# Performance work log

Hardware: AMD Instinct MI355X
Metric: run time of the kernel (lower is better)

## Reference

```python
import jax, jax.numpy as jnp
import numpy as np
import math

B, S, D = 2, 2048, 1024
H = 16
HD = D // H
FFN = 2048
E = 8
TOP_K = 2
CAP_FACTOR = 1.25
EPS = 1e-6
BASE = 10000.0
CAP = max(math.ceil(B * S * TOP_K * CAP_FACTOR / E), 1)  # 1280


def setup_inputs() -> dict:
    key = jax.random.key(0)
    ks = jax.random.split(key, 6)
    sd = 0.02
    return {
        "x": jax.random.normal(ks[0], (B, S, D), jnp.float32),
        "g1": jnp.ones((D,), jnp.float32),
        "w_qkv": jax.random.normal(ks[1], (D, 3 * D), jnp.float32) * sd,
        "w_o": jax.random.normal(ks[2], (D, D), jnp.float32) * sd,
        "g2": jnp.ones((D,), jnp.float32),
        "w_router": jax.random.normal(ks[3], (D, E), jnp.float32) * sd,
        "w1": jax.random.normal(ks[4], (E, D, FFN), jnp.float32) * sd,
        "w2": jax.random.normal(ks[5], (E, FFN, D), jnp.float32) * sd,
    }


def _rmsnorm(x, w):
    rms = jax.lax.rsqrt(jnp.mean(x * x, axis=-1, keepdims=True) + EPS)
    return w * x * rms


def _rope(x, cos, sin):
    # x: [b,h,s,hd]; consecutive pairs (2i, 2i+1) form complex numbers
    xr = x[..., 0::2]
    xi = x[..., 1::2]
    c = cos[None, None]  # [1,1,s,hd/2]
    s_ = sin[None, None]
    out_r = xr * c - xi * s_
    out_i = xr * s_ + xi * c
    return jnp.stack([out_r, out_i], axis=-1).reshape(x.shape)


def _mha(x, w_qkv, w_o):
    b, s, d = x.shape
    qkv = x @ w_qkv
    q, k, v = jnp.split(qkv, 3, axis=-1)
    to_heads = lambda z: z.reshape(b, s, H, HD).transpose(0, 2, 1, 3)
    q, k, v = to_heads(q), to_heads(k), to_heads(v)
    # rotary embedding
    theta = BASE ** (-2.0 * (jnp.arange(HD // 2, dtype=jnp.float32) / HD))
    freqs = jnp.arange(s, dtype=jnp.float32)[:, None] * theta[None, :]  # [s,hd/2]
    cos, sin = jnp.cos(freqs), jnp.sin(freqs)
    q = _rope(q, cos, sin)
    k = _rope(k, cos, sin)
    scores = jnp.einsum('bhqd,bhkd->bhqk', q, k) / jnp.sqrt(jnp.float32(HD))
    causal = jnp.tril(jnp.ones((s, s), dtype=bool))
    scores = jnp.where(causal, scores, -jnp.inf)
    attn = jax.nn.softmax(scores, axis=-1)
    y = jnp.einsum('bhqk,bhkd->bhqd', attn, v)
    y = y.transpose(0, 2, 1, 3).reshape(b, s, d)
    return y @ w_o


def _moe(x, w_router, w1, w2):
    b, s, d = x.shape
    t = b * s
    xf = x.reshape(t, d)
    logits = xf.astype(jnp.float32) @ w_router.astype(jnp.float32)
    probs = jax.nn.softmax(logits, axis=-1)  # [t,E]
    g, eidx = jax.lax.top_k(probs, TOP_K)  # [t,K]
    fg = g.reshape(t * TOP_K)
    fe = eidx.reshape(t * TOP_K)
    tok_of = jnp.arange(t * TOP_K) // TOP_K
    # per-expert masked gates, then capacity-based top-CAP selection
    masked = jnp.where(fe[None, :] == jnp.arange(E)[:, None], fg[None, :], -jnp.inf)  # [E, t*K]
    vals, idx = jax.lax.top_k(masked, CAP)  # [E, CAP]
    valid = jnp.isfinite(vals)
    gates = jnp.where(valid, vals, 0.0)  # dropped/empty slots get zero gate
    tok = tok_of[idx]  # [E, CAP] token ids (arbitrary for invalid slots, gate 0)
    xe = xf[tok]  # [E, CAP, d]
    h = jax.nn.relu(jnp.einsum('ecd,edf->ecf', xe, w1))
    ye = jnp.einsum('ecf,efd->ecd', h, w2) * gates[..., None]
    y = jnp.zeros_like(xf).at[tok.reshape(-1)].add(ye.reshape(-1, d))
    return y.reshape(b, s, d)


def reference(x, g1, w_qkv, w_o, g2, w_router, w1, w2):
    x = x + _mha(_rmsnorm(x, g1), w_qkv, w_o)
    x = x + _moe(_rmsnorm(x, g2), w_router, w1, w2)
    return x
```

## Files before the change

kernel.cpp:

```cpp
#include <hip/hip_runtime.h>
#include <math.h>


#define B_   2
#define S_   2048
#define D_   1024
#define H_   16
#define HD_  64
#define FFN_ 2048
#define E_   8
#define CAP_ 1280
#define T_   (B_*S_)
#define NSLOT_ 72

typedef unsigned short u16;
typedef __attribute__((ext_vector_type(8))) short     short8;
typedef __attribute__((ext_vector_type(8))) _Float16  half8;
typedef __attribute__((ext_vector_type(4))) _Float16  half4;
typedef __attribute__((ext_vector_type(8))) unsigned short ushort8v;
typedef __attribute__((ext_vector_type(4))) float     f32x4;

__device__ __forceinline__ u16 f2bf(float f) {
  unsigned u = __float_as_uint(f);
  return (u16)((u + 0x7fffu + ((u >> 16) & 1u)) >> 16);
}
__device__ __forceinline__ float bf2f(u16 h) {
  return __uint_as_float(((unsigned)h) << 16);
}
__device__ __forceinline__ u16 f2h(float f) {
  _Float16 h = (_Float16)f;
  return __builtin_bit_cast(u16, h);
}
__device__ __forceinline__ float h2f(u16 b) {
  return (float)__builtin_bit_cast(_Float16, b);
}

__device__ __forceinline__ void cstore(float* p, float v) { *p = v; }
__device__ __forceinline__ void cstore(u16* p, float v)   { *p = f2bf(v); }

__device__ __forceinline__ void glds16(const u16* g, u16* l) {
  __builtin_amdgcn_global_load_lds(
      (const __attribute__((address_space(1))) unsigned int*)g,
      (__attribute__((address_space(3))) unsigned int*)l, 16, 0, 0);
}

__global__ void init_k(int* cnt) {
  if (threadIdx.x < 16) cnt[threadIdx.x] = 0;
}

__global__ __launch_bounds__(256) void rmsnorm_k(const float* __restrict__ x,
                                                 const float* __restrict__ g,
                                                 float* __restrict__ of,
                                                 u16*   __restrict__ ob,
                                                 u16*   __restrict__ ohh,
                                                 u16*   __restrict__ ohl) {
  const int t = blockIdx.x, tid = threadIdx.x;
  const float4 xv = ((const float4*)(x + (size_t)t * D_))[tid];
  float ss = xv.x*xv.x + xv.y*xv.y + xv.z*xv.z + xv.w*xv.w;
  #pragma unroll
  for (int off = 32; off; off >>= 1) ss += __shfl_down(ss, off);
  __shared__ float wsum[4];
  if ((tid & 63) == 0) wsum[tid >> 6] = ss;
  __syncthreads();
  const float tot = wsum[0] + wsum[1] + wsum[2] + wsum[3];
  const float rms = 1.0f / sqrtf(tot * (1.0f / D_) + 1e-6f);
  const float4 gv = ((const float4*)g)[tid];
  float4 o;
  o.x = gv.x * xv.x * rms;
  o.y = gv.y * xv.y * rms;
  o.z = gv.z * xv.z * rms;
  o.w = gv.w * xv.w * rms;
  if (of) ((float4*)(of + (size_t)t * D_))[tid] = o;
  if (ob) {
    ushort4 h;
    h.x = f2bf(o.x); h.y = f2bf(o.y); h.z = f2bf(o.z); h.w = f2bf(o.w);
    ((ushort4*)(ob + (size_t)t * D_))[tid] = h;
  }
  if (ohh) {
    ushort4 hh, hl;
    hh.x = f2h(o.x); hl.x = f2h(o.x - h2f(hh.x));
    hh.y = f2h(o.y); hl.y = f2h(o.y - h2f(hh.y));
    hh.z = f2h(o.z); hl.z = f2h(o.z - h2f(hh.z));
    hh.w = f2h(o.w); hl.w = f2h(o.w - h2f(hh.w));
    ((ushort4*)(ohh + (size_t)t * D_))[tid] = hh;
    ((ushort4*)(ohl + (size_t)t * D_))[tid] = hl;
  }
}

template<bool RESID>
__global__ __launch_bounds__(256) void gemm_split(const u16* __restrict__ Ah,
                                                  const u16* __restrict__ Al,
                                                  const u16* __restrict__ Bh,
                                                  const u16* __restrict__ Bl,
                                                  const float* __restrict__ resid,
                                                  float* __restrict__ C,
                                                  int K, int lda, int ldb, int ldc) {
  __shared__ u16 AsH[128 * 32], AsL[128 * 32];
  __shared__ u16 BsH[128 * 32], BsL[128 * 32];
  const int tid = threadIdx.x;
  const int bm = blockIdx.y, bn = blockIdx.x;
  const int lane = tid & 63, wave = tid >> 6;
  const int wy = wave >> 1, wx = wave & 1;
  const int l15 = lane & 15, lq = lane >> 4;
  f32x4 acc[4][4];
  #pragma unroll
  for (int i = 0; i < 4; ++i)
    #pragma unroll
    for (int j = 0; j < 4; ++j)
      #pragma unroll
      for (int r = 0; r < 4; ++r) acc[i][j][r] = 0.0f;
  const int srow = lane >> 2, skc = (lane & 3) * 8;
  size_t ga[2], gb[2];
  int ldsoff[2];
  #pragma unroll
  for (int c = 0; c < 2; ++c) {
    const int q = wave * 2 + c;
    ga[c] = (size_t)(bm * 128 + q * 16 + srow) * lda + skc;
    gb[c] = (size_t)(bn * 128 + q * 16 + srow) * ldb + skc;
    ldsoff[c] = q * 512 + lane * 8;
  }

  for (int kt = 0; kt < K; kt += 32) {
    __syncthreads();
    #pragma unroll
    for (int c = 0; c < 2; ++c) {
      glds16(Ah + ga[c] + kt, &AsH[ldsoff[c]]);
      glds16(Al + ga[c] + kt, &AsL[ldsoff[c]]);
      glds16(Bh + gb[c] + kt, &BsH[ldsoff[c]]);
      glds16(Bl + gb[c] + kt, &BsL[ldsoff[c]]);
    }
    __syncthreads();
    half8 ah[4], al[4], bh[4], bl[4];
    #pragma unroll
    for (int i = 0; i < 4; ++i) {
      const int row = (wy * 64 + i * 16 + l15) * 32 + lq * 8;
      ah[i] = *(const half8*)&AsH[row];
      al[i] = *(const half8*)&AsL[row];
    }
    #pragma unroll
    for (int j = 0; j < 4; ++j) {
      const int row = (wx * 64 + j * 16 + l15) * 32 + lq * 8;
      bh[j] = *(const half8*)&BsH[row];
      bl[j] = *(const half8*)&BsL[row];
    }
    #pragma unroll
    for (int i = 0; i < 4; ++i)
      #pragma unroll
      for (int j = 0; j < 4; ++j) {
        acc[i][j] = __builtin_amdgcn_mfma_f32_16x16x32_f16(ah[i], bh[j], acc[i][j], 0, 0, 0);
        acc[i][j] = __builtin_amdgcn_mfma_f32_16x16x32_f16(ah[i], bl[j], acc[i][j], 0, 0, 0);
        acc[i][j] = __builtin_amdgcn_mfma_f32_16x16x32_f16(al[i], bh[j], acc[i][j], 0, 0, 0);
      }
  }
  #pragma unroll
  for (int i = 0; i < 4; ++i)
    #pragma unroll
    for (int j = 0; j < 4; ++j)
      #pragma unroll
      for (int r = 0; r < 4; ++r) {
        const int row = bm * 128 + wy * 64 + i * 16 + lq * 4 + r;
        const int col = bn * 128 + wx * 64 + j * 16 + l15;
        float v = acc[i][j][r];
        if (RESID) v += resid[(size_t)row * ldc + col];
        C[(size_t)row * ldc + col] = v;
      }
}

__global__ __launch_bounds__(256) void wsplit_t_k(const float* __restrict__ src,
                                                  u16* __restrict__ dh,
                                                  u16* __restrict__ dl,
                                                  int R, int C) {
  __shared__ float tile[32][33];
  const int tid = threadIdx.x;
  const int r0 = blockIdx.y * 32, c0 = blockIdx.x * 32;
  const int tx = tid & 31, ty = tid >> 5;
  #pragma unroll
  for (int i = 0; i < 4; ++i)
    tile[ty + i * 8][tx] = src[(size_t)(r0 + ty + i * 8) * C + c0 + tx];
  __syncthreads();
  #pragma unroll
  for (int i = 0; i < 4; ++i) {
    const float v = tile[tx][ty + i * 8];
    const u16 hh = f2h(v);
    const size_t o = (size_t)(c0 + ty + i * 8) * R + r0 + tx;
    dh[o] = hh;
    dl[o] = f2h(v - h2f(hh));
  }
}

__global__ __launch_bounds__(256) void ropesplit_k(const float* __restrict__ qkv,
                                                   u16* __restrict__ qhi, u16* __restrict__ qlo,
                                                   u16* __restrict__ khi, u16* __restrict__ klo) {
  const int i = blockIdx.x * 256 + threadIdx.x;
  const int j = i & 31;
  const int h = (i >> 5) & 15;
  const int t = i >> 9;
  const int s = t & (S_ - 1);
  const int b = t >> 11;
  const int bh = b * 16 + h;
  const float theta = (float)pow(10000.0, -(double)j / 32.0);
  const float fr = (float)s * theta;
  const float c = cosf(fr), sn = sinf(fr);
  const float2 q = *(const float2*)(qkv + (size_t)t * 3072 + h * 64 + 2 * j);
  const float2 k = *(const float2*)(qkv + (size_t)t * 3072 + 1024 + h * 64 + 2 * j);
  const float q0 = (q.x * c - q.y * sn) * 0.125f;
  const float q1 = (q.x * sn + q.y * c) * 0.125f;
  const float k0 = k.x * c - k.y * sn;
  const float k1 = k.x * sn + k.y * c;
  const size_t o = ((size_t)bh * S_ + s) * 32 + j;
  const u16 qh0 = f2bf(q0), qh1 = f2bf(q1);
  const u16 kh0 = f2bf(k0), kh1 = f2bf(k1);
  ((unsigned*)qhi)[o] = (unsigned)qh0 | ((unsigned)qh1 << 16);
  ((unsigned*)khi)[o] = (unsigned)kh0 | ((unsigned)kh1 << 16);
  const u16 ql0 = f2bf(q0 - bf2f(qh0)), ql1 = f2bf(q1 - bf2f(qh1));
  const u16 kl0 = f2bf(k0 - bf2f(kh0)), kl1 = f2bf(k1 - bf2f(kh1));
  ((unsigned*)qlo)[o] = (unsigned)ql0 | ((unsigned)ql1 << 16);
  ((unsigned*)klo)[o] = (unsigned)kl0 | ((unsigned)kl1 << 16);
}

__global__ __launch_bounds__(256) void vpack_k(const float* __restrict__ qkv,
                                               u16* __restrict__ vpk) {
  const int kt = blockIdx.x, bh = blockIdx.y;
  const int b = bh >> 4, h = bh & 15;
  const int tid = threadIdx.x;
  u16* dst = vpk + (size_t)(bh * 32 + kt) * 8192;
  #pragma unroll
  for (int i = 0; i < 4; ++i) {
    const int g = i * 256 + tid;
    const int lane = g & 63, n = (g >> 6) & 3, kc = g >> 8;
    const int lq = lane >> 4, l15 = lane & 15;
    const int key = kt * 64 + kc * 16 + lq * 4;
    const int d = n * 16 + l15;
    u16 out[8];
    #pragma unroll
    for (int j = 0; j < 4; ++j) {
      const float v = qkv[(size_t)(b * S_ + key + j) * 3072 + 2048 + h * 64 + d];
      const u16 hh = f2h(v);
      out[j] = hh;
      out[4 + j] = f2h(v - h2f(hh));
    }
    *(ushort8v*)(dst + g * 8) = *(ushort8v*)out;
  }
}

__global__ __launch_bounds__(256, 4) void attn_mfma_k(const u16* __restrict__ qhi,
                                                      const u16* __restrict__ qlo,
                                                      const u16* __restrict__ khi,
                                                      const u16* __restrict__ klo,
                                                      const u16* __restrict__ vpk,
                                                      u16* __restrict__ ahh,
                                                      u16* __restrict__ ahl,
                                                      float* __restrict__ PO,
                                                      float* __restrict__ Pm,
                                                      float* __restrict__ Pl2) {
  __shared__ u16 Kh[64 * 64], Kl[64 * 64];
  __shared__ u16 Vp[8192];
  const int tid = threadIdx.x, lane = tid & 63, wave = tid >> 6;
  const int bi = blockIdx.x;
  int qt, j;
  if (bi < 32)      { qt = 24 + (bi >> 2);        j = bi & 3; }
  else if (bi < 56) { qt = 16 + (bi - 32) / 3;    j = (bi - 32) % 3; }
  else if (bi < 72) { qt = 8 + ((bi - 56) >> 1);  j = (bi - 56) & 1; }
  else              { qt = bi - 72;               j = 0; }
  const int k0 = j * 8;
  const int k1_ = k0 + 8, nk = qt + 1;
  const int k1 = (k1_ < nk) ? k1_ : nk;
  const bool partial = (qt >= 8);
  int slot = 0;
  if (partial)
    slot = (qt < 16) ? (qt - 8) * 2 + j
         : (qt < 24) ? 16 + (qt - 16) * 3 + j
                     : 40 + (qt - 24) * 4 + j;
  const int bh = blockIdx.y;
  const int l15 = lane & 15, lq = lane >> 4;
  const size_t hb = (size_t)bh * S_ * 64;
  const int qrow = qt * 64 + wave * 16 + l15;
  short8 qh[2], ql[2];
  qh[0] = *(const short8*)(qhi + hb + (size_t)qrow * 64 + lq * 8);
  qh[1] = *(const short8*)(qhi + hb + (size_t)qrow * 64 + 32 + lq * 8);
  ql[0] = *(const short8*)(qlo + hb + (size_t)qrow * 64 + lq * 8);
  ql[1] = *(const short8*)(qlo + hb + (size_t)qrow * 64 + 32 + lq * 8);
  f32x4 O[4];
  #pragma unroll
  for (int n = 0; n < 4; ++n)
    #pragma unroll
    for (int r = 0; r < 4; ++r) O[n][r] = 0.0f;
  float m_i = -__builtin_inff(), l_i = 0.0f;

  const int srow0 = tid >> 3,         sc80 = (tid & 7) * 8;
  const int srow1 = (256 + tid) >> 3, sc81 = sc80;
  const int swz0 = srow0 * 64 + (sc80 ^ ((srow0 & 7) << 3));
  const int swz1 = srow1 * 64 + (sc81 ^ ((srow1 & 7) << 3));
  const int vlds = wave * 2048 + lane * 8;
  ushort8v kregH[2], kregL[2], vreg[4];

  auto issue_loads = [&](int kt) {
    const size_t koff0 = hb + (size_t)(kt * 64 + srow0) * 64 + sc80;
    const size_t koff1 = hb + (size_t)(kt * 64 + srow1) * 64 + sc81;
    kregH[0] = *(const ushort8v*)(khi + koff0);
    kregL[0] = *(const ushort8v*)(klo + koff0);
    kregH[1] = *(const ushort8v*)(khi + koff1);
    kregL[1] = *(const ushort8v*)(klo + koff1);
    const u16* vg = vpk + (size_t)(bh * 32 + kt) * 8192 + vlds;
    #pragma unroll
    for (int c = 0; c < 4; ++c)
      vreg[c] = *(const ushort8v*)(vg + c * 512);
  };
  auto write_lds = [&]() {
    *(ushort8v*)&Kh[swz0] = kregH[0];
    *(ushort8v*)&Kl[swz0] = kregL[0];
    *(ushort8v*)&Kh[swz1] = kregH[1];
    *(ushort8v*)&Kl[swz1] = kregL[1];
    #pragma unroll
    for (int c = 0; c < 4; ++c)
      *(ushort8v*)&Vp[vlds + c * 512] = vreg[c];
  };

  issue_loads(k0);
  write_lds();
  __syncthreads();

  for (int kt = k0; kt < k1; ++kt) {
    const bool pf = (kt + 1 < k1);
    if (pf) issue_loads(kt + 1);
    f32x4 sc[4];
    #pragma unroll
    for (int kc = 0; kc < 4; ++kc)
      #pragma unroll
      for (int r = 0; r < 4; ++r) sc[kc][r] = 0.0f;
    __builtin_amdgcn_s_setprio(1);
    #pragma unroll
    for (int kc = 0; kc < 4; ++kc) {
      const int row = kc * 16 + l15;
      const int x = (row & 7) << 3;
      const short8 kb0 = *(const short8*)&Kh[row * 64 + ((lq * 8) ^ x)];
      const short8 kb1 = *(const short8*)&Kh[row * 64 + ((32 + lq * 8) ^ x)];
      const short8 kl0 = *(const short8*)&Kl[row * 64 + ((lq * 8) ^ x)];
      const short8 kl1 = *(const short8*)&Kl[row * 64 + ((32 + lq * 8) ^ x)];
      sc[kc] = __builtin_amdgcn_mfma_f32_16x16x32_bf16(kb0, qh[0], sc[kc], 0, 0, 0);
      sc[kc] = __builtin_amdgcn_mfma_f32_16x16x32_bf16(kb1, qh[1], sc[kc], 0, 0, 0);
      sc[kc] = __builtin_amdgcn_mfma_f32_16x16x32_bf16(kb0, ql[0], sc[kc], 0, 0, 0);
      sc[kc] = __builtin_amdgcn_mfma_f32_16x16x32_bf16(kb1, ql[1], sc[kc], 0, 0, 0);
      sc[kc] = __builtin_amdgcn_mfma_f32_16x16x32_bf16(kl0, qh[0], sc[kc], 0, 0, 0);
      sc[kc] = __builtin_amdgcn_mfma_f32_16x16x32_bf16(kl1, qh[1], sc[kc], 0, 0, 0);
    }
    __builtin_amdgcn_s_setprio(0);
    if (kt == qt) {
      #pragma unroll
      for (int kc = 0; kc < 4; ++kc)
        #pragma unroll
        for (int r = 0; r < 4; ++r)
          if (kc * 16 + lq * 4 + r > wave * 16 + l15) sc[kc][r] = -__builtin_inff();
    }
    float mx = -__builtin_inff();
    #pragma unroll
    for (int kc = 0; kc < 4; ++kc)
      #pragma unroll
      for (int r = 0; r < 4; ++r) mx = fmaxf(mx, sc[kc][r]);
    mx = fmaxf(mx, __shfl_xor(mx, 16));
    mx = fmaxf(mx, __shfl_xor(mx, 32));
    const float mn = fmaxf(m_i, mx);
    const float alpha = __expf(m_i - mn);
    m_i = mn;
    f32x4 p[4];
    float rs = 0.0f;
    #pragma unroll
    for (int kc = 0; kc < 4; ++kc)
      #pragma unroll
      for (int r = 0; r < 4; ++r) { p[kc][r] = __expf(sc[kc][r] - m_i); rs += p[kc][r]; }
    rs += __shfl_xor(rs, 16);
    rs += __shfl_xor(rs, 32);
    l_i = l_i * alpha + rs;
    #pragma unroll
    for (int r = 0; r < 4; ++r) {
      const float alr = __shfl(alpha, lq * 4 + r);
      #pragma unroll
      for (int n = 0; n < 4; ++n) O[n][r] *= alr;
    }
    half4 ph[4], pl[4];
    #pragma unroll
    for (int kc = 0; kc < 4; ++kc)
      #pragma unroll
      for (int r = 0; r < 4; ++r) {
        const _Float16 hi = (_Float16)p[kc][r];
        ph[kc][r] = hi;
        pl[kc][r] = (_Float16)(p[kc][r] - (float)hi);
      }
    __builtin_amdgcn_s_setprio(1);
    #pragma unroll
    for (int n = 0; n < 4; ++n)
      #pragma unroll
      for (int kc = 0; kc < 4; ++kc) {
        const int g = ((kc * 4 + n) * 64 + lane) * 8;
        const half4 vh = *(const half4*)&Vp[g];
        const half4 vl = *(const half4*)&Vp[g + 4];
        O[n] = __builtin_amdgcn_mfma_f32_16x16x16f16(ph[kc], vh, O[n], 0, 0, 0);
        O[n] = __builtin_amdgcn_mfma_f32_16x16x16f16(ph[kc], vl, O[n], 0, 0, 0);
        O[n] = __builtin_amdgcn_mfma_f32_16x16x16f16(pl[kc], vh, O[n], 0, 0, 0);
      }
    __builtin_amdgcn_s_setprio(0);
    __syncthreads();
    if (pf) write_lds();
    __syncthreads();
  }
  const int b = bh >> 4, h = bh & 15;
  if (!partial) {
    #pragma unroll
    for (int r = 0; r < 4; ++r) {
      const float lr = __shfl(l_i, lq * 4 + r);
      const float inv = 1.0f / lr;
      const int row = qt * 64 + wave * 16 + lq * 4 + r;
      const size_t base = (size_t)(b * S_ + row) * D_ + h * 64 + l15;
      #pragma unroll
      for (int n = 0; n < 4; ++n) {
        const float o = O[n][r] * inv;
        const u16 hh = f2h(o);
        ahh[base + n * 16] = hh;
        ahl[base + n * 16] = f2h(o - h2f(hh));
      }
    }
  } else {
    #pragma unroll
    for (int r = 0; r < 4; ++r) {
      const int lr = wave * 16 + lq * 4 + r;
      const size_t idx = ((size_t)bh * NSLOT_ + slot) * 64 + lr;
      float* po = PO + idx * 64;
      #pragma unroll
      for (int n = 0; n < 4; ++n) po[n * 16 + l15] = O[n][r];
    }
    if (lq == 0) {
      const int lr = wave * 16 + l15;
      const size_t idx = ((size_t)bh * NSLOT_ + slot) * 64 + lr;
      Pm[idx] = m_i; Pl2[idx] = l_i;
    }
  }
}

__global__ __launch_bounds__(256) void attn_combine_k(const float* __restrict__ PO,
                                                      const float* __restrict__ Pm,
                                                      const float* __restrict__ Pl2,
                                                      u16* __restrict__ ahh,
                                                      u16* __restrict__ ahl) {
  const int tid = threadIdx.x;
  const int qt = 8 + blockIdx.x;
  const int bh = blockIdx.y, b = bh >> 4, h = bh & 15;
  const int Cq  = (qt < 16) ? 2 : (qt < 24 ? 3 : 4);
  const int off = (qt < 16) ? (qt - 8) * 2
                : (qt < 24) ? 16 + (qt - 16) * 3
                            : 40 + (qt - 24) * 4;
  const int lr = tid >> 2;
  const int d0 = (tid & 3) * 16;
  float m[4], w[4];
  float M = -__builtin_inff();
  for (int c = 0; c < Cq; ++c) {
    m[c] = Pm[((size_t)bh * NSLOT_ + off + c) * 64 + lr];
    M = fmaxf(M, m[c]);
  }
  float L = 0.0f;
  for (int c = 0; c < Cq; ++c) {
    w[c] = __expf(m[c] - M);
    L += w[c] * Pl2[((size_t)bh * NSLOT_ + off + c) * 64 + lr];
  }
  const float inv = 1.0f / L;
  const int row = qt * 64 + lr;
  const size_t ob = (size_t)(b * S_ + row) * D_ + h * 64 + d0;
  #pragma unroll
  for (int q4 = 0; q4 < 4; ++q4) {
    float v[4] = {0.0f, 0.0f, 0.0f, 0.0f};
    for (int c = 0; c < Cq; ++c) {
      const float4 o = *(const float4*)(PO +
          (((size_t)bh * NSLOT_ + off + c) * 64 + lr) * 64 + d0 + q4 * 4);
      v[0] = fmaf(w[c], o.x, v[0]);
      v[1] = fmaf(w[c], o.y, v[1]);
      v[2] = fmaf(w[c], o.z, v[2]);
      v[3] = fmaf(w[c], o.w, v[3]);
    }
    ushort4 hh, hl;
    u16* ph = (u16*)&hh;
    u16* pl = (u16*)&hl;
    #pragma unroll
    for (int z = 0; z < 4; ++z) {
      const float vn = v[z] * inv;
      ph[z] = f2h(vn);
      pl[z] = f2h(vn - h2f(ph[z]));
    }
    *(ushort4*)(ahh + ob + q4 * 4) = hh;
    *(ushort4*)(ahl + ob + q4 * 4) = hl;
  }
}

__global__ __launch_bounds__(256) void router_k(const float* __restrict__ y2,
                                                const float* __restrict__ wr,
                                                int*   __restrict__ cnt,
                                                int*   __restrict__ tok_e,
                                                float* __restrict__ tok_g,
                                                int*   __restrict__ tok_p,
                                                int*   __restrict__ etok) {
  __shared__ int   lcnt[8];
  __shared__ int   base[8];
  __shared__ int   le[64];
  __shared__ float lg[64];
  __shared__ int   lpo[64];
  const int wave = threadIdx.x >> 6, lane = threadIdx.x & 63;
  const int t0 = blockIdx.x * 32;
  if (threadIdx.x < 8) lcnt[threadIdx.x] = 0;
  __syncthreads();
  for (int i = 0; i < 8; ++i) {
    const int r = wave * 8 + i;
    const float* xr = y2 + (size_t)(t0 + r) * D_;
    float acc[8];
    #pragma unroll
    for (int e = 0; e < 8; ++e) acc[e] = 0.0f;
    for (int c = 0; c < 16; ++c) {
      const float xv = xr[c * 64 + lane];
      const float* w = wr + (size_t)(c * 64 + lane) * 8;
      #pragma unroll
      for (int e = 0; e < 8; ++e) acc[e] = fmaf(xv, w[e], acc[e]);
    }
    #pragma unroll
    for (int off = 32; off; off >>= 1)
      #pragma unroll
      for (int e = 0; e < 8; ++e) acc[e] += __shfl_down(acc[e], off);
    if (lane == 0) {
      float mx = acc[0];
      #pragma unroll
      for (int e = 1; e < 8; ++e) mx = fmaxf(mx, acc[e]);
      float ex[8], sum = 0.0f;
      #pragma unroll
      for (int e = 0; e < 8; ++e) { ex[e] = expf(acc[e] - mx); sum += ex[e]; }
      int e1 = 0;
      #pragma unroll
      for (int e = 1; e < 8; ++e) if (acc[e] > acc[e1]) e1 = e;
      int e2 = (e1 == 0) ? 1 : 0;
      #pragma unroll
      for (int e = 0; e < 8; ++e) if (e != e1 && acc[e] > acc[e2]) e2 = e;
      le[2 * r]     = e1;  lg[2 * r]     = ex[e1] / sum;
      le[2 * r + 1] = e2;  lg[2 * r + 1] = ex[e2] / sum;
    }
  }
  __syncthreads();
  if (threadIdx.x < 64) lpo[threadIdx.x] = atomicAdd(&lcnt[le[threadIdx.x]], 1);
  __syncthreads();
  if (threadIdx.x < 8)
    base[threadIdx.x] = atomicAdd(&cnt[threadIdx.x], lcnt[threadIdx.x]);
  __syncthreads();
  if (threadIdx.x < 64) {
    const int t = t0 + (threadIdx.x >> 1);
    const int e = le[threadIdx.x];
    int p = base[e] + lpo[threadIdx.x];
    if (p < CAP_) etok[e * CAP_ + p] = t; else p = -1;
    tok_e[2 * t0 + threadIdx.x] = e;
    tok_g[2 * t0 + threadIdx.x] = lg[threadIdx.x];
    tok_p[2 * t0 + threadIdx.x] = p;
  }
}

__global__ __launch_bounds__(256) void gather_k(const u16* __restrict__ y2b,
                                                const int* __restrict__ etok,
                                                const int* __restrict__ cnt,
                                                u16* __restrict__ xe) {
  const int e = blockIdx.y, pos = blockIdx.x, tid = threadIdx.x;
  const int n = min(cnt[e], CAP_);
  ushort4* dst = (ushort4*)(xe + (size_t)(e * CAP_ + pos) * D_) + tid;
  if (pos < n) {
    const int t = etok[e * CAP_ + pos];
    *dst = ((const ushort4*)(y2b + (size_t)t * D_))[tid];
  } else {
    *dst = make_ushort4(0, 0, 0, 0);
  }
}

template<typename OT, bool RELU>
__global__ __launch_bounds__(256) void gemm_bt(const u16* __restrict__ A,
                                               const u16* __restrict__ Bt,
                                               OT* __restrict__ C,
                                               int M, int N, int K,
                                               int lda, int ldb, int ldc,
                                               long sAz, long sBz, long sCz) {
  __shared__ u16 As[2][128 * 32];
  __shared__ u16 Bs[2][128 * 32];
  const int tid = threadIdx.x;
  A  += (size_t)blockIdx.z * sAz;
  Bt += (size_t)blockIdx.z * sBz;
  C  += (size_t)blockIdx.z * sCz;
  const int bm = blockIdx.y, bn = blockIdx.x;
  const int lane = tid & 63, wave = tid >> 6;
  const int wy = wave >> 1, wx = wave & 1;
  const int l15 = lane & 15, lq = lane >> 4;
  f32x4 acc[4][4];
  #pragma unroll
  for (int i = 0; i < 4; ++i)
    #pragma unroll
    for (int j = 0; j < 4; ++j)
      #pragma unroll
      for (int r = 0; r < 4; ++r) acc[i][j][r] = 0.0f;
  const int srow = lane >> 2, skc = (lane & 3) * 8;
  size_t ga[2], gb[2];
  int ldsoff[2];
  #pragma unroll
  for (int c = 0; c < 2; ++c) {
    const int q = wave * 2 + c;
    ga[c] = (size_t)(bm * 128 + q * 16 + srow) * lda + skc;
    gb[c] = (size_t)(bn * 128 + q * 16 + srow) * ldb + skc;
    ldsoff[c] = q * 512 + lane * 8;
  }
  auto stage = [&](int buf, int kt) {
    #pragma unroll
    for (int c = 0; c < 2; ++c) {
      glds16(A  + ga[c] + kt, &As[buf][ldsoff[c]]);
      glds16(Bt + gb[c] + kt, &Bs[buf][ldsoff[c]]);
    }
  };

  stage(0, 0);
  __syncthreads();
  int cur = 0;
  for (int kt = 0; kt < K; kt += 32) {
    if (kt + 32 < K) stage(cur ^ 1, kt + 32);
    short8 a[4], b[4];
    #pragma unroll
    for (int i = 0; i < 4; ++i)
      a[i] = *(const short8*)&As[cur][(wy * 64 + i * 16 + l15) * 32 + lq * 8];
    #pragma unroll
    for (int j = 0; j < 4; ++j)
      b[j] = *(const short8*)&Bs[cur][(wx * 64 + j * 16 + l15) * 32 + lq * 8];
    #pragma unroll
    for (int i = 0; i < 4; ++i)
      #pragma unroll
      for (int j = 0; j < 4; ++j)
        acc[i][j] = __builtin_amdgcn_mfma_f32_16x16x32_bf16(a[i], b[j], acc[i][j], 0, 0, 0);
    __syncthreads();
    cur ^= 1;
  }
  #pragma unroll
  for (int i = 0; i < 4; ++i)
    #pragma unroll
    for (int j = 0; j < 4; ++j)
      #pragma unroll
      for (int r = 0; r < 4; ++r) {
        const int row = bm * 128 + wy * 64 + i * 16 + lq * 4 + r;
        const int col = bn * 128 + wx * 64 + j * 16 + l15;
        float v = acc[i][j][r];
        if (RELU) v = fmaxf(v, 0.0f);
        cstore(C + (size_t)row * ldc + col, v);
      }
}

__global__ __launch_bounds__(256) void transpose_bf_k(const float* __restrict__ src,
                                                      u16* __restrict__ dst,
                                                      int R, int C) {
  __shared__ float tile[32][33];
  const int tid = threadIdx.x;
  const size_t zoff = (size_t)blockIdx.z * R * C;
  const int r0 = blockIdx.y * 32, c0 = blockIdx.x * 32;
  const int tx = tid & 31, ty = tid >> 5;
  #pragma unroll
  for (int i = 0; i < 4; ++i)
    tile[ty + i * 8][tx] = src[zoff + (size_t)(r0 + ty + i * 8) * C + c0 + tx];
  __syncthreads();
  #pragma unroll
  for (int i = 0; i < 4; ++i)
    dst[zoff + (size_t)(c0 + ty + i * 8) * R + r0 + tx] = f2bf(tile[tx][ty + i * 8]);
}

__global__ __launch_bounds__(256) void combine_k(const float* __restrict__ x2,
                                                 const float* __restrict__ ye,
                                                 const int*   __restrict__ tok_e,
                                                 const float* __restrict__ tok_g,
                                                 const int*   __restrict__ tok_p,
                                                 float* __restrict__ out) {
  const int t = blockIdx.x, tid = threadIdx.x;
  float4 v = ((const float4*)(x2 + (size_t)t * D_))[tid];
  #pragma unroll
  for (int r = 0; r < 2; ++r) {
    const int p = tok_p[2 * t + r];
    if (p >= 0) {
      const int e = tok_e[2 * t + r];
      const float g = tok_g[2 * t + r];
      const float4 y = ((const float4*)(ye + (size_t)(e * CAP_ + p) * D_))[tid];
      v.x = fmaf(g, y.x, v.x);
      v.y = fmaf(g, y.y, v.y);
      v.z = fmaf(g, y.z, v.z);
      v.w = fmaf(g, y.w, v.w);
    }
  }
  ((float4*)(out + (size_t)t * D_))[tid] = v;
}

extern "C" void kernel_launch(void* const* d_in, const int* in_sizes, int n_in,
                              void* d_out, int out_size, void* d_ws, size_t ws_size,
                              hipStream_t stream) {
  const float* x    = (const float*)d_in[0];
  const float* g1   = (const float*)d_in[1];
  const float* wqkv = (const float*)d_in[2];
  const float* wo   = (const float*)d_in[3];
  const float* g2   = (const float*)d_in[4];
  const float* wr   = (const float*)d_in[5];
  const float* w1   = (const float*)d_in[6];
  const float* w2   = (const float*)d_in[7];
  float* out = (float*)d_out;
  char* ws = (char*)d_ws;
  const size_t MB = 1ull << 20;

  u16*   y1hh  = (u16*)  (ws + 0);
  u16*   y1hl  = (u16*)  (ws + 8 * MB);
  u16*   ahh   = (u16*)  (ws + 16 * MB);
  u16*   ahl   = (u16*)  (ws + 24 * MB);
  u16*   hbf   = (u16*)  (ws + 0);
  float* qkv   = (float*)(ws + 40 * MB);
  float* PO    = (float*)(ws + 40 * MB);
  float* Pm    = (float*)(ws + 78 * MB);
  float* Pl2   = (float*)(ws + 79 * MB);
  u16*   xe    = (u16*)  (ws + 40 * MB);
  float* x2    = (float*)(ws + 88 * MB);
  float* y2    = (float*)(ws + 104 * MB);
  u16*   y2b   = (u16*)  (ws + 120 * MB);
  u16*   w1t   = (u16*)  (ws + 128 * MB);
  u16*   w2t   = (u16*)  (ws + 160 * MB);
  float* ye    = (float*)(ws + 192 * MB);
  u16*   wqh   = (u16*)  (ws + 192 * MB);
  u16*   wql   = (u16*)  (ws + 198 * MB);
  u16*   khi   = (u16*)  (ws + 192 * MB);
  u16*   klo   = (u16*)  (ws + 200 * MB);
  u16*   vpk   = (u16*)  (ws + 208 * MB);
  u16*   woh   = (u16*)  (ws + 224 * MB);
  u16*   wol   = (u16*)  (ws + 226 * MB);
  int*   cnt   = (int*)  (ws + 232 * MB);
  int*   tok_e = cnt + 16;
  float* tok_g = (float*)(tok_e + 2 * T_);
  int*   tok_p = (int*)  (tok_g + 2 * T_);
  int*   etok  = tok_p + 2 * T_;

  init_k<<<1, 64, 0, stream>>>(cnt);
  transpose_bf_k<<<dim3(FFN_/32, D_/32, E_), 256, 0, stream>>>(w1, w1t, D_, FFN_);
  transpose_bf_k<<<dim3(D_/32, FFN_/32, E_), 256, 0, stream>>>(w2, w2t, FFN_, D_);
  wsplit_t_k<<<dim3(3*D_/32, D_/32), 256, 0, stream>>>(wqkv, wqh, wql, D_, 3*D_);
  wsplit_t_k<<<dim3(D_/32, D_/32), 256, 0, stream>>>(wo, woh, wol, D_, D_);

  rmsnorm_k<<<T_, 256, 0, stream>>>(x, g1, (float*)nullptr, (u16*)nullptr, y1hh, y1hl);
  gemm_split<false><<<dim3(3 * D_ / 128, T_ / 128), 256, 0, stream>>>(
      y1hh, y1hl, wqh, wql, nullptr, qkv, D_, D_, D_, 3 * D_);
  ropesplit_k<<<T_ * H_ * 32 / 256, 256, 0, stream>>>(qkv, y1hh, y1hl, khi, klo);
  vpack_k<<<dim3(S_ / 64, B_ * H_), 256, 0, stream>>>(qkv, vpk);
  attn_mfma_k<<<dim3(80, B_ * H_), 256, 0, stream>>>(
      y1hh, y1hl, khi, klo, vpk, ahh, ahl, PO, Pm, Pl2);
  attn_combine_k<<<dim3(24, B_ * H_), 256, 0, stream>>>(PO, Pm, Pl2, ahh, ahl);
  gemm_split<true><<<dim3(D_ / 128, T_ / 128), 256, 0, stream>>>(
      ahh, ahl, woh, wol, x, x2, D_, D_, D_, D_);
  rmsnorm_k<<<T_, 256, 0, stream>>>(x2, g2, y2, y2b, (u16*)nullptr, (u16*)nullptr);
  router_k<<<T_ / 32, 256, 0, stream>>>(y2, wr, cnt, tok_e, tok_g, tok_p, etok);
  gather_k<<<dim3(CAP_, E_), 256, 0, stream>>>(y2b, etok, cnt, xe);
  gemm_bt<u16, true><<<dim3(FFN_/128, CAP_/128, E_), 256, 0, stream>>>(
      xe, w1t, hbf, CAP_, FFN_, D_, D_, D_, FFN_,
      (long)CAP_ * D_, (long)FFN_ * D_, (long)CAP_ * FFN_);
  gemm_bt<float, false><<<dim3(D_/128, CAP_/128, E_), 256, 0, stream>>>(
      hbf, w2t, ye, CAP_, D_, FFN_, FFN_, FFN_, D_,
      (long)CAP_ * FFN_, (long)D_ * FFN_, (long)CAP_ * D_);
  combine_k<<<T_, 256, 0, stream>>>(x2, ye, tok_e, tok_g, tok_p, out);
}
```

Measured before the change: 644.7 us.

## Load attention K fragments directly from global, double-buffer V, remap GEMM blocks per XCD

Result: slower. 730.4 us (+13.3%).

```diff
diff --git a/kernel.cpp b/kernel.cpp
--- a/kernel.cpp
+++ b/kernel.cpp
@@ -98,7 +98,10 @@
   __shared__ u16 AsH[128 * 32], AsL[128 * 32];
   __shared__ u16 BsH[128 * 32], BsL[128 * 32];
   const int tid = threadIdx.x;
-  const int bm = blockIdx.y, bn = blockIdx.x;
+  const int nwg = gridDim.x * gridDim.y;
+  int bid = blockIdx.y * gridDim.x + blockIdx.x;
+  bid = (bid & 7) * (nwg >> 3) + (bid >> 3);
+  const int bm = bid / gridDim.x, bn = bid % gridDim.x;
   const int lane = tid & 63, wave = tid >> 6;
   const int wy = wave >> 1, wx = wave & 1;
   const int l15 = lane & 15, lq = lane >> 4;
@@ -243,7 +246,7 @@
   }
 }
 
-__global__ __launch_bounds__(256, 4) void attn_mfma_k(const u16* __restrict__ qhi,
+__global__ __launch_bounds__(256, 3) void attn_mfma_k(const u16* __restrict__ qhi,
                                                       const u16* __restrict__ qlo,
                                                       const u16* __restrict__ khi,
                                                       const u16* __restrict__ klo,
@@ -253,8 +256,7 @@
                                                       float* __restrict__ PO,
                                                       float* __restrict__ Pm,
                                                       float* __restrict__ Pl2) {
-  __shared__ u16 Kh[64 * 64], Kl[64 * 64];
-  __shared__ u16 Vp[8192];
+  __shared__ u16 Vp[2][8192];
   const int tid = threadIdx.x, lane = tid & 63, wave = tid >> 6;
   const int bi = blockIdx.x;
   int qt, j;
@@ -287,42 +289,37 @@
     for (int r = 0; r < 4; ++r) O[n][r] = 0.0f;
   float m_i = -__builtin_inff(), l_i = 0.0f;
 
-  const int srow0 = tid >> 3,         sc80 = (tid & 7) * 8;
-  const int srow1 = (256 + tid) >> 3, sc81 = sc80;
-  const int swz0 = srow0 * 64 + (sc80 ^ ((srow0 & 7) << 3));
-  const int swz1 = srow1 * 64 + (sc81 ^ ((srow1 & 7) << 3));
   const int vlds = wave * 2048 + lane * 8;
-  ushort8v kregH[2], kregL[2], vreg[4];
-
-  auto issue_loads = [&](int kt) {
-    const size_t koff0 = hb + (size_t)(kt * 64 + srow0) * 64 + sc80;
-    const size_t koff1 = hb + (size_t)(kt * 64 + srow1) * 64 + sc81;
-    kregH[0] = *(const ushort8v*)(khi + koff0);
-    kregL[0] = *(const ushort8v*)(klo + koff0);
-    kregH[1] = *(const ushort8v*)(khi + koff1);
-    kregL[1] = *(const ushort8v*)(klo + koff1);
+  ushort8v vreg[4];
+  auto issue_v = [&](int kt) {
     const u16* vg = vpk + (size_t)(bh * 32 + kt) * 8192 + vlds;
     #pragma unroll
     for (int c = 0; c < 4; ++c)
       vreg[c] = *(const ushort8v*)(vg + c * 512);
   };
-  auto write_lds = [&]() {
-    *(ushort8v*)&Kh[swz0] = kregH[0];
-    *(ushort8v*)&Kl[swz0] = kregL[0];
-    *(ushort8v*)&Kh[swz1] = kregH[1];
-    *(ushort8v*)&Kl[swz1] = kregL[1];
+  auto write_v = [&](int buf) {
     #pragma unroll
     for (int c = 0; c < 4; ++c)
-      *(ushort8v*)&Vp[vlds + c * 512] = vreg[c];
+      *(ushort8v*)&Vp[buf][vlds + c * 512] = vreg[c];
   };
 
-  issue_loads(k0);
-  write_lds();
-  __syncthreads();
+  issue_v(k0);
+  write_v(0);
+  __syncthreads();
+  int cur = 0;
 
   for (int kt = k0; kt < k1; ++kt) {
     const bool pf = (kt + 1 < k1);
-    if (pf) issue_loads(kt + 1);
+    short8 kb[4][2], klr[4][2];
+    #pragma unroll
+    for (int kc = 0; kc < 4; ++kc) {
+      const size_t ro = hb + (size_t)(kt * 64 + kc * 16 + l15) * 64 + lq * 8;
+      kb[kc][0]  = *(const short8*)(khi + ro);
+      kb[kc][1]  = *(const short8*)(khi + ro + 32);
+      klr[kc][0] = *(const short8*)(klo + ro);
+      klr[kc][1] = *(const short8*)(klo + ro + 32);
+    }
+    if (pf) issue_v(kt + 1);
     f32x4 sc[4];
     #pragma unroll
     for (int kc = 0; kc < 4; ++kc)
@@ -331,18 +328,12 @@
     __builtin_amdgcn_s_setprio(1);
     #pragma unroll
     for (int kc = 0; kc < 4; ++kc) {
-      const int row = kc * 16 + l15;
-      const int x = (row & 7) << 3;
-      const short8 kb0 = *(const short8*)&Kh[row * 64 + ((lq * 8) ^ x)];
-      const short8 kb1 = *(const short8*)&Kh[row * 64 + ((32 + lq * 8) ^ x)];
-      const short8 kl0 = *(const short8*)&Kl[row * 64 + ((lq * 8) ^ x)];
-      const short8 kl1 = *(const short8*)&Kl[row * 64 + ((32 + lq * 8) ^ x)];
-      sc[kc] = __builtin_amdgcn_mfma_f32_16x16x32_bf16(kb0, qh[0], sc[kc], 0, 0, 0);
-      sc[kc] = __builtin_amdgcn_mfma_f32_16x16x32_bf16(kb1, qh[1], sc[kc], 0, 0, 0);
-      sc[kc] = __builtin_amdgcn_mfma_f32_16x16x32_bf16(kb0, ql[0], sc[kc], 0, 0, 0);
-      sc[kc] = __builtin_amdgcn_mfma_f32_16x16x32_bf16(kb1, ql[1], sc[kc], 0, 0, 0);
-      sc[kc] = __builtin_amdgcn_mfma_f32_16x16x32_bf16(kl0, qh[0], sc[kc], 0, 0, 0);
-      sc[kc] = __builtin_amdgcn_mfma_f32_16x16x32_bf16(kl1, qh[1], sc[kc], 0, 0, 0);
+      sc[kc] = __builtin_amdgcn_mfma_f32_16x16x32_bf16(kb[kc][0],  qh[0], sc[kc], 0, 0, 0);
+      sc[kc] = __builtin_amdgcn_mfma_f32_16x16x32_bf16(kb[kc][1],  qh[1], sc[kc], 0, 0, 0);
+      sc[kc] = __builtin_amdgcn_mfma_f32_16x16x32_bf16(kb[kc][0],  ql[0], sc[kc], 0, 0, 0);
+      sc[kc] = __builtin_amdgcn_mfma_f32_16x16x32_bf16(kb[kc][1],  ql[1], sc[kc], 0, 0, 0);
+      sc[kc] = __builtin_amdgcn_mfma_f32_16x16x32_bf16(klr[kc][0], qh[0], sc[kc], 0, 0, 0);
+      sc[kc] = __builtin_amdgcn_mfma_f32_16x16x32_bf16(klr[kc][1], qh[1], sc[kc], 0, 0, 0);
     }
     __builtin_amdgcn_s_setprio(0);
     if (kt == qt) {
@@ -392,16 +383,16 @@
       #pragma unroll
       for (int kc = 0; kc < 4; ++kc) {
         const int g = ((kc * 4 + n) * 64 + lane) * 8;
-        const half4 vh = *(const half4*)&Vp[g];
-        const half4 vl = *(const half4*)&Vp[g + 4];
+        const half4 vh = *(const half4*)&Vp[cur][g];
+        const half4 vl = *(const half4*)&Vp[cur][g + 4];
         O[n] = __builtin_amdgcn_mfma_f32_16x16x16f16(ph[kc], vh, O[n], 0, 0, 0);
         O[n] = __builtin_amdgcn_mfma_f32_16x16x16f16(ph[kc], vl, O[n], 0, 0, 0);
         O[n] = __builtin_amdgcn_mfma_f32_16x16x16f16(pl[kc], vh, O[n], 0, 0, 0);
       }
     __builtin_amdgcn_s_setprio(0);
+    if (pf) write_v(cur ^ 1);
     __syncthreads();
-    if (pf) write_lds();
-    __syncthreads();
+    cur ^= 1;
   }
   const int b = bh >> 4, h = bh & 15;
   if (!partial) {
@@ -583,7 +574,10 @@
   A  += (size_t)blockIdx.z * sAz;
   Bt += (size_t)blockIdx.z * sBz;
   C  += (size_t)blockIdx.z * sCz;
-  const int bm = blockIdx.y, bn = blockIdx.x;
+  const int nwg = gridDim.x * gridDim.y;
+  int bid = blockIdx.y * gridDim.x + blockIdx.x;
+  bid = (bid & 7) * (nwg >> 3) + (bid >> 3);
+  const int bm = bid / gridDim.x, bn = bid % gridDim.x;
   const int lane = tid & 63, wave = tid >> 6;
   const int wy = wave >> 1, wx = wave & 1;
   const int l15 = lane & 15, lq = lane >> 4;
```
